# Performance work log

Measured on AMD Instinct MI355X. Metric: run time of the kernel, lower is better.

The kernel has to match this reference:

```python
import jax, jax.numpy as jnp
import numpy as np
import math

D_MODEL = 128
N_HEADS = 8
D_K = D_MODEL // N_HEADS
D_FF = 512
N_LAYERS = 3
N_BUCKETS = 32
EPS = 1e-5
NEG_INF = -1e9
SCALE = 1.0 / math.sqrt(D_K)


def _hier_adj_np(N, L=8):
    # deterministic hierarchical edges from ExpanderGraphBuilder.build_hierarchical_edges
    stride = max(1, int(math.sqrt(N / L)))
    layer_size = N // L if L <= N else 1
    A = np.zeros((N, N), dtype=np.float32)
    for l in range(min(L, N)):
        start = l * layer_size
        end = min(start + layer_size, N)
        for i in range(start, end):
            A[i, max(start, i - stride):min(end, i + stride + 1)] = 1.0
            A[i, i] = 0.0
    return np.maximum(A, A.T)


def _build_mask(h, depot_idx=0):
    # h: (B,N,D). Returns additive mask (B,N+1,N+1) incl. global node.
    B, N, _ = h.shape
    k = min(max(1, math.ceil(math.log2(N))), N - 1)
    sq = jnp.sum(h * h, axis=-1)
    d2 = sq[:, :, None] + sq[:, None, :] - 2.0 * jnp.einsum('bnd,bmd->bnm', h, h)
    d2 = d2 + jnp.where(jnp.eye(N, dtype=bool), jnp.inf, 0.0)
    _, knn_idx = jax.lax.top_k(-d2, k)  # (B,N,k) nearest neighbors
    b_ix = jnp.arange(B)[:, None, None]
    i_ix = jnp.arange(N)[None, :, None]
    adj = jnp.zeros((B, N, N), dtype=h.dtype).at[b_ix, i_ix, knn_idx].set(1.0)
    adj = jnp.maximum(adj, adj.transpose(0, 2, 1))  # symmetrize knn
    adj = jnp.maximum(adj, jnp.asarray(_hier_adj_np(N))[None])
    adj = adj.at[:, depot_idx, :].set(1.0)
    adj = adj.at[:, :, depot_idx].set(1.0)
    adj = jnp.maximum(adj, jnp.eye(N, dtype=h.dtype)[None])
    full = jnp.ones((B, N + 1, N + 1), dtype=h.dtype).at[:, :N, :N].set(adj)
    return jnp.where(full > 0, 0.0, NEG_INF).astype(h.dtype)


def _inorm(x, w, b):
    # InstanceNorm1d over node dim per channel (x: (B,N1,D))
    mu = jnp.mean(x, axis=1, keepdims=True)
    var = jnp.mean(jnp.square(x - mu), axis=1, keepdims=True)
    return (x - mu) * jax.lax.rsqrt(var + EPS) * w + b


def _ega_layer(hg, bucket, mask, Wq, Wk, Wv, Wo, emb, W1, b1, W2, b2, n1w, n1b, n2w, n2b):
    B, N1, D = hg.shape
    heads = lambda x: x.reshape(B, N1, N_HEADS, D_K).transpose(0, 2, 1, 3)
    Q, K, V = heads(hg @ Wq.T), heads(hg @ Wk.T), heads(hg @ Wv.T)
    scores = jnp.einsum('bhnd,bhmd->bhnm', Q, K) * SCALE
    # rel_scores[b,h,i,j] = <Q[b,h,i], emb[bucket[b,i,j], h]> : contract with the
    # 32-entry table first, then gather - same math, no (B,H,N,N,Dk) intermediate.
    qe = jnp.einsum('bhnd,khd->bhnk', Q, emb.reshape(N_BUCKETS, N_HEADS, D_K))
    rel = jnp.take_along_axis(qe, jnp.broadcast_to(bucket[:, None], (B, N_HEADS, N1, N1)), axis=3)
    attn = jax.nn.softmax(scores + rel + mask[:, None], axis=-1)
    ctx = jnp.einsum('bhnm,bhmd->bhnd', attn, V).transpose(0, 2, 1, 3).reshape(B, N1, D)
    h1 = _inorm(hg + ctx @ Wo.T, n1w, n1b)
    ffn = jax.nn.relu(h1 @ W1.T + b1) @ W2.T + b2
    return _inorm(h1 + ffn, n2w, n2b)


def _forward(coords, in_W, in_b, gnode, Wq, Wk, Wv, Wo, emb, W1, b1, W2, b2,
             n1_w, n1_b, n2_w, n2_b, out_W, out_b):
    B, N, _ = coords.shape
    h = coords @ in_W.T + in_b
    g = jnp.broadcast_to(gnode, (B, 1, D_MODEL)).astype(h.dtype)
    # distance buckets over coords extended with the global node at (0,0)
    coords_ext = jnp.concatenate([coords, jnp.zeros((B, 1, 2), coords.dtype)], axis=1)
    diff = coords_ext[:, :, None, :] - coords_ext[:, None, :, :]
    dist = jax.lax.stop_gradient(jnp.sqrt(jnp.sum(diff * diff, axis=-1)))
    bucket = jnp.clip((dist * N_BUCKETS).astype(jnp.int32), 0, N_BUCKETS - 1)  # (B,N+1,N+1)
    pools = []
    for l in range(N_LAYERS):
        g = g + h.mean(axis=1, keepdims=True)
        hg = jnp.concatenate([h, g], axis=1)
        mask = _build_mask(jax.lax.stop_gradient(h))  # torch builds adj via .item(): detached
        hg = _ega_layer(hg, bucket, mask, Wq[l], Wk[l], Wv[l], Wo[l], emb[l],
                        W1[l], b1[l], W2[l], b2[l], n1_w[l], n1_b[l], n2_w[l], n2_b[l])
        h, g = hg[:, :N], hg[:, N:]
        pools.append(h.mean(axis=1))
    p_multi = jnp.stack(pools, axis=1).mean(axis=1)
    E_static = (h + p_multi[:, None, :]) @ out_W.T + out_b
    return E_static, p_multi


def setup_inputs():
    key = jax.random.key(0)
    ks = jax.random.split(key, 24)
    B, N, L = 2, 1024, N_LAYERS
    def nrm(k, shape, s=0.05):
        return jax.random.normal(k, shape, dtype=jnp.float32) * s
    return {
        'coords': jax.random.uniform(ks[0], (B, N, 2), dtype=jnp.float32),
        'in_W': nrm(ks[1], (D_MODEL, 2), 0.5),
        'in_b': nrm(ks[2], (D_MODEL,)),
        'gnode': nrm(ks[3], (1, 1, D_MODEL), 0.2),
        'Wq': nrm(ks[4], (L, D_MODEL, D_MODEL)),
        'Wk': nrm(ks[5], (L, D_MODEL, D_MODEL)),
        'Wv': nrm(ks[6], (L, D_MODEL, D_MODEL)),
        'Wo': nrm(ks[7], (L, D_MODEL, D_MODEL)),
        'emb': nrm(ks[8], (L, N_BUCKETS, N_HEADS * D_K)),
        'W1': nrm(ks[9], (L, D_FF, D_MODEL)),
        'b1': nrm(ks[10], (L, D_FF)),
        'W2': nrm(ks[11], (L, D_MODEL, D_FF)),
        'b2': nrm(ks[12], (L, D_MODEL)),
        'n1_w': jnp.ones((L, D_MODEL), jnp.float32) + nrm(ks[13], (L, D_MODEL)),
        'n1_b': nrm(ks[14], (L, D_MODEL)),
        'n2_w': jnp.ones((L, D_MODEL), jnp.float32) + nrm(ks[15], (L, D_MODEL)),
        'n2_b': nrm(ks[16], (L, D_MODEL)),
        'out_W': nrm(ks[17], (D_MODEL, D_MODEL)),
        'out_b': nrm(ks[18], (D_MODEL,)),
    }


def reference(coords, in_W, in_b, gnode, Wq, Wk, Wv, Wo, emb, W1, b1, W2, b2,
              n1_w, n1_b, n2_w, n2_b, out_W, out_b):
    return _forward(coords, in_W, in_b, gnode, Wq, Wk, Wv, Wo, emb, W1, b1, W2, b2,
                    n1_w, n1_b, n2_w, n2_b, out_W, out_b)
```

## Files before the change

### kernel.cpp

```cpp
#include <hip/hip_runtime.h>

#define BB 2
#define NN 1024
#define N1 1025
#define DM 128
#define NH 8
#define DK 16
#define DFF 512
#define NBUK 32
#define NLAYERS 3
#define KNN_K 10
#define ADJW 17
#define BSTR 1088
#define NSPLIT 8
#define BIGF 3.0e38f
#define SM_OFF 24.0f

#define PWQ_OFF 0
#define PWK_OFF 49152
#define PWV_OFF 98304
#define PWO_OFF 147456
#define PW1_OFF 196608
#define PW2_OFF 393216
#define PWOUT_OFF 589824
#define PWQE_OFF 606208
#define PW_TOT 704512

#define PBLK 344
#define NBNODE 1024
#define EBLK (NBNODE + BB)
#define BBLK 8713

#define KSEL_BLK 512
#define QKV_GX 33
#define QKV_BLK (QKV_GX * 40)
#define OSUM_N (BB * NH * N1 * 16)
#define LSUM_N (BB * NH * N1)
#define STAT_N (BB * DM)
#define ZTOT (OSUM_N + LSUM_N + 2 * STAT_N)

typedef __attribute__((ext_vector_type(8))) short bf8;
typedef __attribute__((ext_vector_type(4))) float f4;
typedef unsigned short u16;
typedef unsigned int u32;

__device__ __forceinline__ u16 f2bf(float x) {
  unsigned u = __float_as_uint(x);
  return (u16)((u + 0x7fff + ((u >> 16) & 1)) >> 16);
}
__device__ __forceinline__ float bf2f(u16 u) {
  return __uint_as_float(((unsigned)u) << 16);
}
__device__ __forceinline__ bf8 mk8(ushort4 a, ushort4 b) {
  bf8 r;
  r[0] = (short)a.x; r[1] = (short)a.y; r[2] = (short)a.z; r[3] = (short)a.w;
  r[4] = (short)b.x; r[5] = (short)b.y; r[6] = (short)b.z; r[7] = (short)b.w;
  return r;
}

__global__ __launch_bounds__(256) void init_kernel(
    const float* __restrict__ coords, const float* __restrict__ inW,
    const float* __restrict__ inb, const float* __restrict__ gnode,
    const float* __restrict__ Wq, const float* __restrict__ Wk,
    const float* __restrict__ Wv, const float* __restrict__ Wo,
    const float* __restrict__ W1, const float* __restrict__ W2,
    const float* __restrict__ oW, const float* __restrict__ emb,
    u16* __restrict__ PH, u16* __restrict__ PL,
    float* __restrict__ X, u16* __restrict__ XH, u16* __restrict__ XM,
    u16* __restrict__ XL, unsigned char* __restrict__ buckp) {
  int blk = blockIdx.x;
  if (blk < PBLK) {
    int idx = blk * 256 + threadIdx.x;
    if (idx >= 88064) return;
    if (idx >= 75776) {
      int rel = idx - 75776;
      int lane = rel & 63, g = rel >> 6;
      int ks = g & 3, nt = g >> 2;
      int n = nt * 16 + (lane & 15);
      int k = ks * 32 + (lane >> 4) * 8;
      int l = n >> 8; int c = n & 255; int h = c >> 5, bk = c & 31;
      const float* e = emb + ((size_t)l * NBUK + bk) * DM + h * DK;
      const float* wq = Wq + ((size_t)l * DM + h * DK) * DM;
      u16* ph = PH + (size_t)idx * 8;
      u16* pl = PL + (size_t)idx * 8;
      #pragma unroll
      for (int q = 0; q < 8; ++q) {
        float s = 0.f;
        #pragma unroll
        for (int d = 0; d < DK; ++d) s += e[d] * wq[(size_t)d * DM + k + q];
        u16 hh = f2bf(s);
        ph[q] = hh;
        pl[q] = f2bf(s - bf2f(hh));
      }
      return;
    }
    const float* W; int rel, Kdim;
    if (idx < 24576) {
      int seg = idx / 6144; rel = idx % 6144; Kdim = 128;
      W = seg == 0 ? Wq : seg == 1 ? Wk : seg == 2 ? Wv : Wo;
    } else if (idx < 49152) { rel = idx - 24576; Kdim = 128; W = W1; }
    else if (idx < 73728)   { rel = idx - 49152; Kdim = 512; W = W2; }
    else                    { rel = idx - 73728; Kdim = 128; W = oW; }
    int lane = rel & 63;
    int g = rel >> 6;
    int ksteps = Kdim >> 5;
    int ks = g % ksteps, nt = g / ksteps;
    int n = nt * 16 + (lane & 15);
    int k = ks * 32 + (lane >> 4) * 8;
    const float* p = W + (size_t)n * Kdim + k;
    u16* ph = PH + (size_t)idx * 8;
    u16* pl = PL + (size_t)idx * 8;
    #pragma unroll
    for (int q = 0; q < 8; ++q) {
      float x = p[q];
      u16 hh = f2bf(x);
      ph[q] = hh;
      pl[q] = f2bf(x - bf2f(hh));
    }
    return;
  }
  if (blk < PBLK + EBLK) {
    int eb = blk - PBLK;
    if (eb >= NBNODE) {
      int b = eb - NBNODE;
      int t = threadIdx.x;
      if (t >= 128) return;
      int lane = t & 63;
      float sx = 0.f, sy = 0.f;
      for (int n = lane; n < NN; n += 64) {
        float2 c = *(const float2*)(coords + (size_t)(b * NN + n) * 2);
        sx += c.x; sy += c.y;
      }
      #pragma unroll
      for (int o = 1; o < 64; o <<= 1) { sx += __shfl_xor(sx, o); sy += __shfl_xor(sy, o); }
      float mx = sx * (1.0f / NN), my = sy * (1.0f / NN);
      int d = t;
      size_t id = ((size_t)b * N1 + NN) * DM + d;
      float v = gnode[d] + inb[d] + mx * inW[d * 2 + 0] + my * inW[d * 2 + 1];
      X[id] = v;
      u16 hh = f2bf(v); float r1 = v - bf2f(hh);
      u16 mm = f2bf(r1);
      XH[id] = hh; XM[id] = mm; XL[id] = f2bf(r1 - bf2f(mm));
      return;
    }
    int idx = eb * 256 + threadIdx.x;
    if (idx >= BB * NN * DM) return;
    int d = idx % DM; int r = idx / DM; int n = r % NN; int b = r / NN;
    float cx = coords[(b * NN + n) * 2 + 0], cy = coords[(b * NN + n) * 2 + 1];
    size_t id = ((size_t)b * N1 + n) * DM + d;
    float v = cx * inW[d * 2 + 0] + cy * inW[d * 2 + 1] + inb[d];
    X[id] = v;
    u16 hh = f2bf(v); float r1 = v - bf2f(hh);
    u16 mm = f2bf(r1);
    XH[id] = hh; XM[id] = mm; XL[id] = f2bf(r1 - bf2f(mm));
    return;
  }
  int idx = (blk - PBLK - EBLK) * 256 + threadIdx.x;
  if (idx >= BB * N1 * BSTR) return;
  int j = idx % BSTR; int r = idx / BSTR; int i = r % N1; int b = r / N1;
  unsigned char v = 0;
  if (j < N1) {
    float xi = 0.f, yi = 0.f, xj = 0.f, yj = 0.f;
    if (i < NN) { xi = coords[(b * NN + i) * 2]; yi = coords[(b * NN + i) * 2 + 1]; }
    if (j < NN) { xj = coords[(b * NN + j) * 2]; yj = coords[(b * NN + j) * 2 + 1]; }
    float dx = xi - xj, dy = yi - yj;
    float dist = sqrtf(dx * dx + dy * dy);
    int bu = (int)(dist * 32.0f);
    bu = bu < 0 ? 0 : (bu > 31 ? 31 : bu);
    v = (unsigned char)bu;
  }
  buckp[idx] = v;
}

__global__ __launch_bounds__(256) void gram_kernel(
    const u16* __restrict__ XH, const u16* __restrict__ XM, const u16* __restrict__ XL,
    unsigned long long* __restrict__ adj, float* __restrict__ d2) {
  __shared__ __align__(16) u16 AsH[32][72];
  __shared__ __align__(16) u16 AsM[32][72];
  __shared__ __align__(16) u16 AsL[32][72];
  __shared__ __align__(16) u16 BsH[64][72];
  __shared__ __align__(16) u16 BsM[64][72];
  __shared__ __align__(16) u16 BsL[64][72];
  __shared__ float sqS[64];
  int b = blockIdx.z;
  int m0 = blockIdx.x * 32, n0 = blockIdx.y * 64;
  size_t boff = (size_t)b * N1;
  int t = threadIdx.x;

  {
    int flat = blockIdx.x + 32 * (blockIdx.y + 16 * blockIdx.z);
    int tid = flat * 256 + t;
    if (tid < BB * N1 * ADJW) adj[tid] = 0ull;
  }

  int lane = t & 63, w = t >> 6;
  int wm = (w >> 1) * 16, wn = (w & 1) * 32;
  int quad = lane >> 4, r16 = lane & 15;

  f4 acc0 = {0.f, 0.f, 0.f, 0.f}, acc1 = {0.f, 0.f, 0.f, 0.f};
  int ar = t >> 3, as_ = (t & 7) * 8;
  int br = t >> 2, bs_ = (t & 3) * 16;
  int sqrow = t >> 2, sqk = (t & 3) * 16;
  float mySq = 0.f;

  for (int k0 = 0; k0 < DM; k0 += 64) {
    {
      size_t src = (boff + m0 + ar) * DM + k0 + as_;
      *(bf8*)&AsH[ar][as_] = *(const bf8*)(XH + src);
      *(bf8*)&AsM[ar][as_] = *(const bf8*)(XM + src);
      *(bf8*)&AsL[ar][as_] = *(const bf8*)(XL + src);
    }
    {
      size_t src = (boff + n0 + br) * DM + k0 + bs_;
      *(bf8*)&BsH[br][bs_] = *(const bf8*)(XH + src);
      *(bf8*)&BsH[br][bs_ + 8] = *(const bf8*)(XH + src + 8);
      *(bf8*)&BsM[br][bs_] = *(const bf8*)(XM + src);
      *(bf8*)&BsM[br][bs_ + 8] = *(const bf8*)(XM + src + 8);
      *(bf8*)&BsL[br][bs_] = *(const bf8*)(XL + src);
      *(bf8*)&BsL[br][bs_ + 8] = *(const bf8*)(XL + src + 8);
    }
    __syncthreads();
    #pragma unroll
    for (int ks = 0; ks < 64; ks += 16) {
      int seg = (quad & 1) * 8;
      bf8 aHM = *(const bf8*)((quad < 2) ? &AsH[wm + r16][ks + seg] : &AsM[wm + r16][ks + seg]);
      bf8 aHL = *(const bf8*)((quad < 2) ? &AsH[wm + r16][ks + seg] : &AsL[wm + r16][ks + seg]);
      #pragma unroll
      for (int tt = 0; tt < 2; ++tt) {
        int nr = wn + tt * 16 + r16;
        bf8 bH = *(const bf8*)&BsH[nr][ks + seg];
        bf8 bM = *(const bf8*)&BsM[nr][ks + seg];
        bf8 b3 = *(const bf8*)((quad < 2) ? &BsL[nr][ks + seg] : &BsH[nr][ks + seg]);
        f4& a = tt ? acc1 : acc0;
        a = __builtin_amdgcn_mfma_f32_16x16x32_bf16(aHM, bH, a, 0, 0, 0);
        a = __builtin_amdgcn_mfma_f32_16x16x32_bf16(aHM, bM, a, 0, 0, 0);
        a = __builtin_amdgcn_mfma_f32_16x16x32_bf16(aHL, b3, a, 0, 0, 0);
      }
    }
    #pragma unroll
    for (int half = 0; half < 2; ++half) {
      bf8 hv = *(const bf8*)&BsH[sqrow][sqk + half * 8];
      bf8 mv = *(const bf8*)&BsM[sqrow][sqk + half * 8];
      bf8 lv = *(const bf8*)&BsL[sqrow][sqk + half * 8];
      #pragma unroll
      for (int q = 0; q < 8; ++q) {
        float x = (bf2f((u16)hv[q]) + bf2f((u16)mv[q])) + bf2f((u16)lv[q]);
        mySq += x * x;
      }
    }
    __syncthreads();
  }
  mySq += __shfl_xor(mySq, 1);
  mySq += __shfl_xor(mySq, 2);
  if ((t & 3) == 0) sqS[sqrow] = mySq;
  __syncthreads();

  #pragma unroll
  for (int tt = 0; tt < 2; ++tt) {
    f4 a = tt ? acc1 : acc0;
    int nl = wn + tt * 16 + r16;
    int n = n0 + nl;
    float sj = sqS[nl];
    #pragma unroll
    for (int reg = 0; reg < 4; ++reg) {
      int m = m0 + wm + quad * 4 + reg;
      float v = (m == n) ? BIGF : (sj - 2.f * a[reg]);
      d2[((size_t)b * NN + m) * NN + n] = v;
    }
  }
}

__global__ __launch_bounds__(256) void knnqkv_kernel(
    const float* __restrict__ d2, unsigned long long* __restrict__ adj,
    const u16* __restrict__ AH, const u16* __restrict__ AL,
    const u16* __restrict__ Pbase_H, const u16* __restrict__ Pbase_L,
    size_t offQ, size_t offK, size_t offV, size_t offE,
    u16* __restrict__ QH, u16* __restrict__ QL,
    u16* __restrict__ KH, u16* __restrict__ KL, u16* __restrict__ Vbf,
    float* __restrict__ qe_all, float* __restrict__ zbuf, int M) {
  __shared__ float dd[4][NN];
  {
    int ztid = blockIdx.x * 256 + threadIdx.x;
    if (ztid < ZTOT) zbuf[ztid] = 0.f;
  }
  int blk = blockIdx.x;
  if (blk < KSEL_BLK) {
    int b = blk / (NN / 4);
    int i0 = (blk % (NN / 4)) * 4;
    int t = threadIdx.x, lane = t & 63, w = t >> 6;

    const float4* src = (const float4*)(d2 + ((size_t)b * NN + i0) * NN);
    float4* dst = (float4*)&dd[0][0];
    #pragma unroll
    for (int x = 0; x < 4; ++x) dst[t + x * 256] = src[t + x * 256];
    __syncthreads();

    int i = i0 + w;
    for (int it = 0; it < KNN_K; ++it) {
      float bv = BIGF; int bi = 0x3fffffff;
      for (int j = lane; j < NN; j += 64) {
        float v = dd[w][j];
        if (v < bv) { bv = v; bi = j; }
      }
      #pragma unroll
      for (int o = 1; o < 64; o <<= 1) {
        float ov = __shfl_xor(bv, o); int oi = __shfl_xor(bi, o);
        if (ov < bv || (ov == bv && oi < bi)) { bv = ov; bi = oi; }
      }
      if (lane == 0) {
        dd[w][bi] = BIGF;
        atomicOr(&adj[((size_t)b * N1 + i) * ADJW + (bi >> 6)], 1ull << (bi & 63));
        atomicOr(&adj[((size_t)b * N1 + bi) * ADJW + (i >> 6)], 1ull << (i & 63));
      }
    }
    return;
  }
  int rel = blk - KSEL_BLK;
  int gx = rel % QKV_GX;
  int y = rel / QKV_GX;
  int z, nt;
  if (y < 8) { z = 0; nt = y; }
  else if (y < 16) { z = 1; nt = y - 8; }
  else if (y < 24) { z = 2; nt = y - 16; }
  else { z = 3; nt = y - 24; }
  size_t woff = z == 0 ? offQ : (z == 1 ? offK : (z == 2 ? offV : offE));
  const u16* PH = Pbase_H + woff;
  const u16* PL = Pbase_L + woff;
  int lane = threadIdx.x & 63;
  int quad = lane >> 4, r16 = lane & 15;
  int mt = gx * 4 + (threadIdx.x >> 6);
  f4 acc = {0.f, 0.f, 0.f, 0.f};
  int m0 = mt * 16;
  int mrow = m0 + r16; if (mrow >= M) mrow = M - 1;
  const u16* aph = AH + (size_t)mrow * DM + quad * 8;
  const u16* apl = AL + (size_t)mrow * DM + quad * 8;
  const u16* ph = PH + ((size_t)nt * 4 * 64 + lane) * 8;
  const u16* pl = PL + ((size_t)nt * 4 * 64 + lane) * 8;
  #pragma unroll
  for (int ks = 0; ks < 4; ++ks) {
    bf8 aH = *(const bf8*)(aph);
    bf8 aL = *(const bf8*)(apl);
    aph += 32; apl += 32;
    bf8 bH = *(const bf8*)(ph + (size_t)ks * 512);
    bf8 bL = *(const bf8*)(pl + (size_t)ks * 512);
    acc = __builtin_amdgcn_mfma_f32_16x16x32_bf16(aH, bH, acc, 0, 0, 0);
    acc = __builtin_amdgcn_mfma_f32_16x16x32_bf16(aH, bL, acc, 0, 0, 0);
    acc = __builtin_amdgcn_mfma_f32_16x16x32_bf16(aL, bH, acc, 0, 0, 0);
  }
  if (m0 >= M) return;
  int n = nt * 16 + r16;
  #pragma unroll
  for (int reg = 0; reg < 4; ++reg) {
    int m = m0 + quad * 4 + reg;
    if (m >= M) continue;
    float v = acc[reg];
    if (z == 3) {
      int b = m / N1, nr = m % N1;
      int h = n >> 5, bk = n & 31;
      qe_all[(((size_t)b * NH + h) * N1 + nr) * 32 + bk] = v;
      continue;
    }
    size_t oi = (size_t)m * DM + n;
    if (z == 0) {
      float sv = v * 0.25f;
      u16 hh = f2bf(sv);
      QH[oi] = hh;
      QL[oi] = f2bf(sv - bf2f(hh));
    } else if (z == 1) {
      u16 hh = f2bf(v);
      KH[oi] = hh;
      KL[oi] = f2bf(v - bf2f(hh));
    } else {
      Vbf[oi] = f2bf(v);
    }
  }
}

__global__ __launch_bounds__(256) void gemm_wo_kernel(
    const float* __restrict__ Osum, const float* __restrict__ lsum,
    const u16* __restrict__ PH, const u16* __restrict__ PL,
    const float* __restrict__ res, float* __restrict__ outF,
    float* __restrict__ sumY, float* __restrict__ sumY2, int M) {
  __shared__ float sA[2][16], sQ[2][16];
  int t = threadIdx.x;
  if (t < 32) {
    sA[t >> 4][t & 15] = 0.f;
    sQ[t >> 4][t & 15] = 0.f;
  }
  __syncthreads();
  int lane = t & 63;
  int quad = lane >> 4, r16 = lane & 15;
  int mt = blockIdx.x * 4 + (t >> 6), nt = blockIdx.y;
  f4 acc = {0.f, 0.f, 0.f, 0.f};
  int m0 = mt * 16;
  int mrow = m0 + r16; if (mrow >= M) mrow = M - 1;
  int b = mrow / N1, nr = mrow % N1;
  const u16* ph = PH + ((size_t)nt * 4 * 64 + lane) * 8;
  const u16* pl = PL + ((size_t)nt * 4 * 64 + lane) * 8;
  #pragma unroll
  for (int ks = 0; ks < 4; ++ks) {
    int k = ks * 32 + quad * 8;
    int h = k >> 4, d0 = k & 15;
    size_t base = (size_t)(b * NH + h) * N1 + nr;
    float inv = 1.0f / lsum[base];
    const float* op = Osum + base * 16 + d0;
    bf8 aH, aL;
    #pragma unroll
    for (int j = 0; j < 8; ++j) {
      float v = op[j] * inv;
      u16 hh = f2bf(v);
      aH[j] = (short)hh;
      aL[j] = (short)f2bf(v - bf2f(hh));
    }
    bf8 bH = *(const bf8*)(ph + (size_t)ks * 512);
    bf8 bL = *(const bf8*)(pl + (size_t)ks * 512);
    acc = __builtin_amdgcn_mfma_f32_16x16x32_bf16(aH, bH, acc, 0, 0, 0);
    acc = __builtin_amdgcn_mfma_f32_16x16x32_bf16(aH, bL, acc, 0, 0, 0);
    acc = __builtin_amdgcn_mfma_f32_16x16x32_bf16(aL, bH, acc, 0, 0, 0);
  }
  int n = nt * 16 + r16;
  if (m0 < M) {
    #pragma unroll
    for (int reg = 0; reg < 4; ++reg) {
      int m = m0 + quad * 4 + reg;
      if (m < M) {
        float v = acc[reg] + res[(size_t)m * DM + n];
        outF[(size_t)m * DM + n] = v;
        int mb2 = m / N1;
        atomicAdd(&sA[mb2][r16], v);
        atomicAdd(&sQ[mb2][r16], v * v);
      }
    }
  }
  __syncthreads();
  if (t < 32) {
    int bb = t >> 4, d = nt * 16 + (t & 15);
    atomicAdd(&sumY[bb * DM + d], sA[bb][t & 15]);
    atomicAdd(&sumY2[bb * DM + d], sQ[bb][t & 15]);
  }
}

__global__ __launch_bounds__(256) void gemm_w1_kernel(
    const float* __restrict__ Yb, const float* __restrict__ sumY,
    const float* __restrict__ sumY2, const float* __restrict__ n1w,
    const float* __restrict__ n1b,
    const u16* __restrict__ PH, const u16* __restrict__ PL,
    const float* __restrict__ bias,
    u16* __restrict__ outH, u16* __restrict__ outL, int M) {
  __shared__ float muS[STAT_N], scvS[STAT_N], shS[STAT_N];
  int t = threadIdx.x;
  {
    float mu = sumY[t] * (1.0f / N1);
    float var = sumY2[t] * (1.0f / N1) - mu * mu;
    int d = t & (DM - 1);
    muS[t] = mu;
    scvS[t] = rsqrtf(var + 1e-5f) * n1w[d];
    shS[t] = n1b[d];
  }
  __syncthreads();
  int lane = t & 63;
  int quad = lane >> 4, r16 = lane & 15;
  int mt = blockIdx.x * 4 + (t >> 6), nt = blockIdx.y;
  f4 acc = {0.f, 0.f, 0.f, 0.f};
  int m0 = mt * 16;
  int mrow = m0 + r16; if (mrow >= M) mrow = M - 1;
  int b = mrow / N1;
  const float* yp = Yb + (size_t)mrow * DM + quad * 8;
  const u16* ph = PH + ((size_t)nt * 4 * 64 + lane) * 8;
  const u16* pl = PL + ((size_t)nt * 4 * 64 + lane) * 8;
  #pragma unroll
  for (int ks = 0; ks < 4; ++ks) {
    int k = ks * 32 + quad * 8;
    bf8 aH, aL;
    #pragma unroll
    for (int half = 0; half < 2; ++half) {
      float4 yv = *(const float4*)(yp + ks * 32 + half * 4);
      float ya[4] = {yv.x, yv.y, yv.z, yv.w};
      #pragma unroll
      for (int q = 0; q < 4; ++q) {
        int sidx = b * DM + k + half * 4 + q;
        float nv = (ya[q] - muS[sidx]) * scvS[sidx] + shS[sidx];
        u16 hh = f2bf(nv);
        aH[half * 4 + q] = (short)hh;
        aL[half * 4 + q] = (short)f2bf(nv - bf2f(hh));
      }
    }
    bf8 bH = *(const bf8*)(ph + (size_t)ks * 512);
    bf8 bL = *(const bf8*)(pl + (size_t)ks * 512);
    acc = __builtin_amdgcn_mfma_f32_16x16x32_bf16(aH, bH, acc, 0, 0, 0);
    acc = __builtin_amdgcn_mfma_f32_16x16x32_bf16(aH, bL, acc, 0, 0, 0);
    acc = __builtin_amdgcn_mfma_f32_16x16x32_bf16(aL, bH, acc, 0, 0, 0);
  }
  if (m0 >= M) return;
  int n = nt * 16 + r16;
  #pragma unroll
  for (int reg = 0; reg < 4; ++reg) {
    int m = m0 + quad * 4 + reg;
    if (m < M) {
      float v = fmaxf(acc[reg] + bias[n], 0.f);
      size_t oi = (size_t)m * DFF + n;
      u16 hh = f2bf(v);
      outH[oi] = hh;
      outL[oi] = f2bf(v - bf2f(hh));
    }
  }
}

__global__ __launch_bounds__(256) void gemm_w2_kernel(
    const u16* __restrict__ AH, const u16* __restrict__ AL,
    const u16* __restrict__ PH, const u16* __restrict__ PL,
    const float* __restrict__ bias, const float* __restrict__ Yb,
    const float* __restrict__ sumY, const float* __restrict__ sumY2,
    const float* __restrict__ n1w, const float* __restrict__ n1b,
    float* __restrict__ outF, int M) {
  __shared__ float muS[STAT_N], scvS[STAT_N], shS[STAT_N];
  int t = threadIdx.x;
  {
    float mu = sumY[t] * (1.0f / N1);
    float var = sumY2[t] * (1.0f / N1) - mu * mu;
    int d = t & (DM - 1);
    muS[t] = mu;
    scvS[t] = rsqrtf(var + 1e-5f) * n1w[d];
    shS[t] = n1b[d];
  }
  __syncthreads();
  int lane = t & 63;
  int quad = lane >> 4, r16 = lane & 15;
  int mt = blockIdx.x * 4 + (t >> 6), nt = blockIdx.y;
  f4 acc = {0.f, 0.f, 0.f, 0.f};
  int m0 = mt * 16;
  int mrow = m0 + r16; if (mrow >= M) mrow = M - 1;
  const u16* aph = AH + (size_t)mrow * DFF + quad * 8;
  const u16* apl = AL + (size_t)mrow * DFF + quad * 8;
  const u16* ph = PH + ((size_t)nt * 16 * 64 + lane) * 8;
  const u16* pl = PL + ((size_t)nt * 16 * 64 + lane) * 8;
  #pragma unroll 4
  for (int ks = 0; ks < 16; ++ks) {
    bf8 aH = *(const bf8*)(aph);
    bf8 aL = *(const bf8*)(apl);
    aph += 32; apl += 32;
    bf8 bH = *(const bf8*)(ph + (size_t)ks * 512);
    bf8 bL = *(const bf8*)(pl + (size_t)ks * 512);
    acc = __builtin_amdgcn_mfma_f32_16x16x32_bf16(aH, bH, acc, 0, 0, 0);
    acc = __builtin_amdgcn_mfma_f32_16x16x32_bf16(aH, bL, acc, 0, 0, 0);
    acc = __builtin_amdgcn_mfma_f32_16x16x32_bf16(aL, bH, acc, 0, 0, 0);
  }
  if (m0 >= M) return;
  int n = nt * 16 + r16;
  #pragma unroll
  for (int reg = 0; reg < 4; ++reg) {
    int m = m0 + quad * 4 + reg;
    if (m < M) {
      int b = m / N1;
      int sidx = b * DM + n;
      float h1 = (Yb[(size_t)m * DM + n] - muS[sidx]) * scvS[sidx] + shS[sidx];
      outF[(size_t)m * DM + n] = acc[reg] + bias[n] + h1;
    }
  }
}

#define CH 64
#define NCH 17
__global__ __launch_bounds__(128) void attn_kernel(
    const u16* __restrict__ QH, const u16* __restrict__ QL,
    const u16* __restrict__ KH, const u16* __restrict__ KL,
    const u16* __restrict__ Vbf, const float* __restrict__ qe_all,
    const unsigned char* __restrict__ buckp, const unsigned long long* __restrict__ adj,
    float* __restrict__ Osum, float* __restrict__ lsum) {
  __shared__ __align__(16) u16 KsHi[2][CH][20];
  __shared__ __align__(16) u16 KsLo[2][CH][20];
  __shared__ __align__(16) u16 Vt[2][DK][68];
  __shared__ __align__(16) u16 Ps[2][16][72];
  __shared__ __align__(16) float qe_s[2][16][36];
  __shared__ u32 maskS[32][6];
  __shared__ unsigned char buckS[2][32][68];

  int qt = blockIdx.x;
  int h = blockIdx.y & 7, b = blockIdx.y >> 3;
  int s = blockIdx.z;
  int c0 = (NCH * s) / NSPLIT, c1 = (NCH * (s + 1)) / NSPLIT;
  int nwm = 2 * (c1 - c0);
  int t = threadIdx.x, lane = t & 63, w = t >> 6;
  int quad = lane >> 4, r16 = lane & 15;
  int i0 = qt * 32;
  int iw = i0 + w * 16;
  int bh = b * NH + h;

  for (int x = t; x < 32 * nwm; x += 128) {
    int rr = x / nwm, ww = x % nwm;
    int gi = i0 + rr; if (gi > NN) gi = NN;
    int W = 2 * c0 + ww;
    u32 v;
    if (gi == 0 || gi == NN) {
      v = 0xffffffffu;
    } else {
      const u32* a32 = (const u32*)(adj + ((size_t)b * N1 + gi) * ADJW);
      v = a32[W];
      int bs = gi & ~127;
      int lo = gi - 11 < bs ? bs : gi - 11;
      int be = bs + 127;
      int hi = gi + 11 > be ? be : gi + 11;
      int aa = lo - 32 * W, bnd = hi - 32 * W;
      if (aa < 0) aa = 0; if (bnd > 31) bnd = 31;
      if (aa <= bnd) v |= (0xffffffffu << aa) & (0xffffffffu >> (31 - bnd));
      if (W == 0) v |= 1u;
      if (W == 32) v |= 1u;
      int dg = gi - 32 * W;
      if (dg >= 0 && dg < 32) v |= 1u << dg;
    }
    if (W == 32) v &= 1u;
    else if (W == 33) v = 0u;
    maskS[rr][ww] = v;
  }
  #pragma unroll
  for (int e = 0; e < 2; ++e) {
    int x = lane + e * 64;
    int rr = x >> 3, bk = (x & 7) * 4;
    int gi = iw + rr; if (gi > NN) gi = NN;
    f4 v = *(const f4*)(qe_all + (((size_t)b * NH + h) * N1 + gi) * 32 + bk);
    *(f4*)&qe_s[w][rr][bk] = v;
  }
  bf8 qfrag;
  {
    int gi = iw + r16; if (gi > NN) gi = NN;
    const u16* qsrc = (quad < 2 ? QH : QL) + ((size_t)(b * N1 + gi) * DM + h * DK + (quad & 1) * 8);
    qfrag = *(const bf8*)qsrc;
  }

  ushort4 khr[2], klr[2], vvr[2]; u32 bkr[4];
  auto load_chunk = [&](int c) {
    int j0 = c * CH;
    #pragma unroll
    for (int ii = 0; ii < 2; ++ii) {
      int x = t + ii * 128;
      int key = x >> 2, ds = (x & 3) * 4;
      int jg = j0 + key; if (jg > NN) jg = NN;
      size_t src = (size_t)(b * N1 + jg) * DM + h * DK + ds;
      khr[ii] = *(const ushort4*)(KH + src);
      klr[ii] = *(const ushort4*)(KL + src);
      vvr[ii] = *(const ushort4*)(Vbf + src);
    }
    #pragma unroll
    for (int ii = 0; ii < 4; ++ii) {
      int x = t + ii * 128;
      int rr = x >> 4, c4 = (x & 15) * 4;
      int gi = i0 + rr; if (gi > NN) gi = NN;
      bkr[ii] = *(const u32*)(buckp + ((size_t)b * N1 + gi) * BSTR + j0 + c4);
    }
  };
  auto store_chunk = [&](int pb) {
    #pragma unroll
    for (int ii = 0; ii < 2; ++ii) {
      int x = t + ii * 128;
      int key = x >> 2, ds = (x & 3) * 4;
      *(ushort4*)&KsHi[pb][key][ds] = khr[ii];
      *(ushort4*)&KsLo[pb][key][ds] = klr[ii];
      Vt[pb][ds + 0][key] = vvr[ii].x;
      Vt[pb][ds + 1][key] = vvr[ii].y;
      Vt[pb][ds + 2][key] = vvr[ii].z;
      Vt[pb][ds + 3][key] = vvr[ii].w;
    }
    #pragma unroll
    for (int ii = 0; ii < 4; ++ii) {
      int x = t + ii * 128;
      int rr = x >> 4, c4 = (x & 15) * 4;
      *(u32*)&buckS[pb][rr][c4] = bkr[ii];
    }
  };

  f4 Oacc = {0.f, 0.f, 0.f, 0.f};
  float lrun[4] = {0.f, 0.f, 0.f, 0.f};

  load_chunk(c0);
  store_chunk(0);

  for (int c = c0; c < c1; ++c) {
    int pb = (c - c0) & 1;
    bool pf = (c + 1 < c1);
    if (pf) load_chunk(c + 1);
    __syncthreads();

    f4 S[4];
    #pragma unroll
    for (int tt = 0; tt < 4; ++tt) {
      int key = tt * 16 + r16;
      int off = (quad & 1) * 8;
      bf8 bhv = mk8(*(const ushort4*)&KsHi[pb][key][off], *(const ushort4*)&KsHi[pb][key][off + 4]);
      bf8 blv = mk8(*(const ushort4*)&KsLo[pb][key][off], *(const ushort4*)&KsLo[pb][key][off + 4]);
      f4 z = {0.f, 0.f, 0.f, 0.f};
      z = __builtin_amdgcn_mfma_f32_16x16x32_bf16(qfrag, bhv, z, 0, 0, 0);
      z = __builtin_amdgcn_mfma_f32_16x16x32_bf16(qfrag, blv, z, 0, 0, 0);
      S[tt] = z;
    }

    #pragma unroll
    for (int rg = 0; rg < 4; ++rg) {
      int rowb = w * 16 + quad * 4 + rg;
      u32 mw0 = maskS[rowb][2 * (c - c0)];
      u32 mw1 = maskS[rowb][2 * (c - c0) + 1];
      float ps = 0.f;
      #pragma unroll
      for (int tt = 0; tt < 4; ++tt) {
        u32 mword = (tt & 2) ? mw1 : mw0;
        int bit = (tt & 1) * 16 + r16;
        int bk = buckS[pb][rowb][tt * 16 + r16] & 31;
        float rel = qe_s[w][quad * 4 + rg][bk];
        float sc = S[tt][rg] + rel;
        sc += ((mword >> bit) & 1u) ? 0.f : -1.0e9f;
        float p = __expf(sc - SM_OFF);
        ps += p;
        Ps[w][quad * 4 + rg][tt * 16 + r16] = f2bf(p);
      }
      #pragma unroll
      for (int o = 1; o < 16; o <<= 1) ps += __shfl_xor(ps, o);
      lrun[rg] += ps;
    }
    #pragma unroll
    for (int half = 0; half < 2; ++half) {
      bf8 pa = *(const bf8*)&Ps[w][r16][half * 32 + quad * 8];
      bf8 vb = mk8(*(const ushort4*)&Vt[pb][r16][half * 32 + quad * 8],
                   *(const ushort4*)&Vt[pb][r16][half * 32 + quad * 8 + 4]);
      Oacc = __builtin_amdgcn_mfma_f32_16x16x32_bf16(pa, vb, Oacc, 0, 0, 0);
    }

    if (pf) store_chunk(pb ^ 1);
  }

  #pragma unroll
  for (int rg = 0; rg < 4; ++rg) {
    int gi = i0 + w * 16 + quad * 4 + rg;
    if (gi < N1) {
      size_t base = (size_t)bh * N1 + gi;
      atomicAdd(&Osum[base * 16 + r16], Oacc[rg]);
      if (r16 == 0) atomicAdd(&lsum[base], lrun[rg]);
    }
  }
}

__global__ void inorm_kernel(float* __restrict__ X, const float* __restrict__ w,
                             const float* __restrict__ b_, float* __restrict__ pool,
                             int do_g, u16* __restrict__ oH, u16* __restrict__ oM,
                             u16* __restrict__ oL) {
  int d = blockIdx.x; int bb = blockIdx.y; int lane = threadIdx.x;
  float g_old = X[((size_t)bb * N1 + NN) * DM + d];
  float s = 0.f;
  for (int n = lane; n < N1; n += 64) s += X[((size_t)bb * N1 + n) * DM + d];
  #pragma unroll
  for (int o = 1; o < 64; o <<= 1) s += __shfl_xor(s, o);
  float mu = s * (1.0f / N1);
  float v = 0.f;
  for (int n = lane; n < N1; n += 64) {
    float tt = X[((size_t)bb * N1 + n) * DM + d] - mu;
    v += tt * tt;
  }
  #pragma unroll
  for (int o = 1; o < 64; o <<= 1) v += __shfl_xor(v, o);
  float var = v * (1.0f / N1);
  float scv = rsqrtf(var + 1e-5f) * w[d];
  float sh = b_[d];
  for (int n = lane; n < N1; n += 64) {
    size_t id = ((size_t)bb * N1 + n) * DM + d;
    float nv = (X[id] - mu) * scv + sh;
    X[id] = nv;
    if (oH) {
      u16 hh = f2bf(nv); float r1 = nv - bf2f(hh);
      u16 mm = f2bf(r1);
      oH[id] = hh;
      oM[id] = mm;
      if (oL) oL[id] = f2bf(r1 - bf2f(mm));
    }
  }
  if (lane == 0) {
    float hmean = ((s - g_old) * (1.0f / NN) - mu) * scv + sh;
    if (pool) pool[bb * DM + d] = hmean;
    if (do_g) X[((size_t)bb * N1 + NN) * DM + d] += hmean;
  }
}

__global__ __launch_bounds__(256) void gemm_final_kernel(
    const float* __restrict__ X, const float* __restrict__ pools,
    const u16* __restrict__ PH, const u16* __restrict__ PL,
    const float* __restrict__ bias, float* __restrict__ out, float* __restrict__ out_pm) {
  int t = threadIdx.x;
  if (blockIdx.x == 0 && blockIdx.y == 0) {
    float pmv = (pools[t] + pools[BB * DM + t] + pools[2 * BB * DM + t]) * (1.0f / 3.0f);
    out_pm[t] = pmv;
  }
  int lane = t & 63;
  int quad = lane >> 4, r16 = lane & 15;
  int mt = blockIdx.x * 4 + (t >> 6), nt = blockIdx.y;
  const int M = BB * NN;
  f4 acc = {0.f, 0.f, 0.f, 0.f};
  int m0 = mt * 16;
  int mrow = m0 + r16; if (mrow >= M) mrow = M - 1;
  int mb = mrow / NN, mn = mrow % NN;
  const float* xp = X + ((size_t)mb * N1 + mn) * DM + quad * 8;
  const float* pp = pools + mb * DM + quad * 8;
  const u16* ph = PH + ((size_t)nt * 4 * 64 + lane) * 8;
  const u16* pl = PL + ((size_t)nt * 4 * 64 + lane) * 8;
  #pragma unroll
  for (int ks = 0; ks < 4; ++ks) {
    bf8 aH, aL;
    #pragma unroll
    for (int half = 0; half < 2; ++half) {
      float4 xv = *(const float4*)(xp + ks * 32 + half * 4);
      float4 p0 = *(const float4*)(pp + ks * 32 + half * 4);
      float4 p1 = *(const float4*)(pp + BB * DM + ks * 32 + half * 4);
      float4 p2 = *(const float4*)(pp + 2 * BB * DM + ks * 32 + half * 4);
      float av[4] = {xv.x + (p0.x + p1.x + p2.x) * (1.0f / 3.0f),
                     xv.y + (p0.y + p1.y + p2.y) * (1.0f / 3.0f),
                     xv.z + (p0.z + p1.z + p2.z) * (1.0f / 3.0f),
                     xv.w + (p0.w + p1.w + p2.w) * (1.0f / 3.0f)};
      #pragma unroll
      for (int q = 0; q < 4; ++q) {
        u16 hh = f2bf(av[q]);
        aH[half * 4 + q] = (short)hh;
        aL[half * 4 + q] = (short)f2bf(av[q] - bf2f(hh));
      }
    }
    bf8 bH = *(const bf8*)(ph + (size_t)ks * 512);
    bf8 bL = *(const bf8*)(pl + (size_t)ks * 512);
    acc = __builtin_amdgcn_mfma_f32_16x16x32_bf16(aH, bH, acc, 0, 0, 0);
    acc = __builtin_amdgcn_mfma_f32_16x16x32_bf16(aH, bL, acc, 0, 0, 0);
    acc = __builtin_amdgcn_mfma_f32_16x16x32_bf16(aL, bH, acc, 0, 0, 0);
  }
  int n = nt * 16 + r16;
  #pragma unroll
  for (int reg = 0; reg < 4; ++reg) {
    int m = m0 + quad * 4 + reg;
    if (m < M) out[(size_t)m * DM + n] = acc[reg] + bias[n];
  }
}

extern "C" void kernel_launch(void* const* d_in, const int* in_sizes, int n_in,
                              void* d_out, int out_size, void* d_ws, size_t ws_size,
                              hipStream_t stream) {
  const float* coords = (const float*)d_in[0];
  const float* inW    = (const float*)d_in[1];
  const float* inb    = (const float*)d_in[2];
  const float* gnode  = (const float*)d_in[3];
  const float* Wq     = (const float*)d_in[4];
  const float* Wk     = (const float*)d_in[5];
  const float* Wv     = (const float*)d_in[6];
  const float* Wo     = (const float*)d_in[7];
  const float* emb    = (const float*)d_in[8];
  const float* W1     = (const float*)d_in[9];
  const float* b1     = (const float*)d_in[10];
  const float* W2     = (const float*)d_in[11];
  const float* b2     = (const float*)d_in[12];
  const float* n1w    = (const float*)d_in[13];
  const float* n1b    = (const float*)d_in[14];
  const float* n2w    = (const float*)d_in[15];
  const float* n2b    = (const float*)d_in[16];
  const float* outW   = (const float*)d_in[17];
  const float* outb   = (const float*)d_in[18];
  float* out = (float*)d_out;

  char* wsp = (char*)d_ws;
  size_t off = 0;
  auto alloc = [&](size_t bytes) -> void* {
    off = (off + 255) & ~(size_t)255;
    void* p = wsp + off;
    off += bytes;
    return p;
  };
  const size_t XB = (size_t)BB * N1 * DM * 4;
  const size_t HB = (size_t)BB * N1 * DM * 2;
  float* X0   = (float*)alloc(XB);
  float* X1   = (float*)alloc(XB);
  float* Yb   = (float*)alloc(XB);
  u16* XH = (u16*)alloc(HB); u16* XM = (u16*)alloc(HB); u16* XL = (u16*)alloc(HB);
  u16* QH = (u16*)alloc(HB); u16* QL = (u16*)alloc(HB);
  u16* KH = (u16*)alloc(HB); u16* KL = (u16*)alloc(HB);
  u16* Vbf = (u16*)alloc(HB);
  u16* FbH = (u16*)alloc((size_t)BB * N1 * DFF * 2);
  u16* FbL = (u16*)alloc((size_t)BB * N1 * DFF * 2);
  unsigned char* buckp = (unsigned char*)alloc((size_t)BB * N1 * BSTR);
  unsigned long long* adj = (unsigned long long*)alloc((size_t)BB * N1 * ADJW * 8);
  float* pools = (float*)alloc((size_t)NLAYERS * BB * DM * 4);
  float* qe_all = (float*)alloc((size_t)BB * NH * N1 * 32 * 4);
  float* zbuf = (float*)alloc((size_t)ZTOT * 4);
  u16* PH = (u16*)alloc((size_t)PW_TOT * 2);
  u16* PL = (u16*)alloc((size_t)PW_TOT * 2);
  float* d2 = (float*)alloc((size_t)BB * NN * NN * 4);

  float* Osum = zbuf;
  float* lsum = zbuf + OSUM_N;
  float* sumY = zbuf + OSUM_N + LSUM_N;
  float* sumY2 = sumY + STAT_N;

  init_kernel<<<PBLK + EBLK + BBLK, 256, 0, stream>>>(
      coords, inW, inb, gnode, Wq, Wk, Wv, Wo, W1, W2, outW, emb,
      PH, PL, X0, XH, XM, XL, buckp);

  float* Xin = X0; float* Xout = X1;
  const int M = BB * N1;
  const int GX = 33;
  for (int l = 0; l < NLAYERS; ++l) {
    gram_kernel<<<dim3(32, 16, BB), 256, 0, stream>>>(XH, XM, XL, adj, d2);

    knnqkv_kernel<<<KSEL_BLK + QKV_BLK, 256, 0, stream>>>(
        d2, adj, XH, XM, PH, PL,
        (size_t)PWQ_OFF + (size_t)l * DM * DM,
        (size_t)PWK_OFF + (size_t)l * DM * DM,
        (size_t)PWV_OFF + (size_t)l * DM * DM,
        (size_t)PWQE_OFF + (size_t)l * 256 * DM,
        QH, QL, KH, KL, Vbf, qe_all, zbuf, M);

    attn_kernel<<<dim3(33, NH * BB, NSPLIT), 128, 0, stream>>>(
        QH, QL, KH, KL, Vbf, qe_all, buckp, adj, Osum, lsum);

    gemm_wo_kernel<<<dim3(GX, 8), 256, 0, stream>>>(
        Osum, lsum, PH + PWO_OFF + (size_t)l * DM * DM, PL + PWO_OFF + (size_t)l * DM * DM,
        Xin, Yb, sumY, sumY2, M);

    gemm_w1_kernel<<<dim3(GX, 32), 256, 0, stream>>>(
        Yb, sumY, sumY2, n1w + l * DM, n1b + l * DM,
        PH + PW1_OFF + (size_t)l * DFF * DM, PL + PW1_OFF + (size_t)l * DFF * DM,
        b1 + l * DFF, FbH, FbL, M);

    gemm_w2_kernel<<<dim3(GX, 8), 256, 0, stream>>>(
        FbH, FbL, PH + PW2_OFF + (size_t)l * DM * DFF, PL + PW2_OFF + (size_t)l * DM * DFF,
        b2 + l * DM, Yb, sumY, sumY2, n1w + l * DM, n1b + l * DM, Xout, M);

    inorm_kernel<<<dim3(DM, BB), 64, 0, stream>>>(Xout, n2w + l * DM, n2b + l * DM,
                                                  pools + (size_t)l * BB * DM, 1,
                                                  XH, XM, XL);

    float* t2 = Xin; Xin = Xout; Xout = t2;
  }

  gemm_final_kernel<<<dim3(32, 8), 256, 0, stream>>>(
      Xin, pools, PH + PWOUT_OFF, PL + PWOUT_OFF, outb, out, out + (size_t)BB * NN * DM);
}
```

Before: 422.3 us.

## Fuse second InstanceNorm statistics into W2 GEMM epilogue and elementwise apply kernel

```diff
diff --git a/kernel.cpp b/kernel.cpp
--- a/kernel.cpp
+++ b/kernel.cpp
@@ -37,7 +37,7 @@
 #define OSUM_N (BB * NH * N1 * 16)
 #define LSUM_N (BB * NH * N1)
 #define STAT_N (BB * DM)
-#define ZTOT (OSUM_N + LSUM_N + 2 * STAT_N)
+#define ZTOT (OSUM_N + LSUM_N + 4 * STAT_N)
 
 typedef __attribute__((ext_vector_type(8))) short bf8;
 typedef __attribute__((ext_vector_type(4))) float f4;
@@ -512,8 +512,10 @@
     const float* __restrict__ bias, const float* __restrict__ Yb,
     const float* __restrict__ sumY, const float* __restrict__ sumY2,
     const float* __restrict__ n1w, const float* __restrict__ n1b,
-    float* __restrict__ outF, int M) {
+    float* __restrict__ outF, float* __restrict__ sumX, float* __restrict__ sumX2,
+    float* __restrict__ gsave, int M) {
   __shared__ float muS[STAT_N], scvS[STAT_N], shS[STAT_N];
+  __shared__ float sA[2][16], sQ[2][16];
   int t = threadIdx.x;
   {
     float mu = sumY[t] * (1.0f / N1);
@@ -522,6 +524,10 @@
     muS[t] = mu;
     scvS[t] = rsqrtf(var + 1e-5f) * n1w[d];
     shS[t] = n1b[d];
+  }
+  if (t < 32) {
+    sA[t >> 4][t & 15] = 0.f;
+    sQ[t >> 4][t & 15] = 0.f;
   }
   __syncthreads();
   int lane = t & 63;
@@ -545,18 +551,53 @@
     acc = __builtin_amdgcn_mfma_f32_16x16x32_bf16(aH, bL, acc, 0, 0, 0);
     acc = __builtin_amdgcn_mfma_f32_16x16x32_bf16(aL, bH, acc, 0, 0, 0);
   }
-  if (m0 >= M) return;
   int n = nt * 16 + r16;
-  #pragma unroll
-  for (int reg = 0; reg < 4; ++reg) {
-    int m = m0 + quad * 4 + reg;
-    if (m < M) {
-      int b = m / N1;
-      int sidx = b * DM + n;
-      float h1 = (Yb[(size_t)m * DM + n] - muS[sidx]) * scvS[sidx] + shS[sidx];
-      outF[(size_t)m * DM + n] = acc[reg] + bias[n] + h1;
-    }
-  }
+  if (m0 < M) {
+    #pragma unroll
+    for (int reg = 0; reg < 4; ++reg) {
+      int m = m0 + quad * 4 + reg;
+      if (m < M) {
+        int b = m / N1, mn2 = m % N1;
+        int sidx = b * DM + n;
+        float h1 = (Yb[(size_t)m * DM + n] - muS[sidx]) * scvS[sidx] + shS[sidx];
+        float v = acc[reg] + bias[n] + h1;
+        outF[(size_t)m * DM + n] = v;
+        atomicAdd(&sA[b][r16], v);
+        atomicAdd(&sQ[b][r16], v * v);
+        if (mn2 == NN) gsave[sidx] = v;
+      }
+    }
+  }
+  __syncthreads();
+  if (t < 32) {
+    int bb = t >> 4, d = nt * 16 + (t & 15);
+    atomicAdd(&sumX[bb * DM + d], sA[bb][t & 15]);
+    atomicAdd(&sumX2[bb * DM + d], sQ[bb][t & 15]);
+  }
+}
+
+__global__ __launch_bounds__(256) void xsplit2_kernel(
+    float* __restrict__ X, const float* __restrict__ sumX, const float* __restrict__ sumX2,
+    const float* __restrict__ gsave, const float* __restrict__ w, const float* __restrict__ b_,
+    float* __restrict__ pool, u16* __restrict__ XH, u16* __restrict__ XM,
+    u16* __restrict__ XL) {
+  int idx = blockIdx.x * 256 + threadIdx.x;
+  if (idx >= BB * N1 * DM) return;
+  int d = idx % DM; int r = idx / DM; int n = r % N1; int b = r / N1;
+  int sidx = b * DM + d;
+  float sx = sumX[sidx];
+  float mu = sx * (1.0f / N1);
+  float var = sumX2[sidx] * (1.0f / N1) - mu * mu;
+  float scv = rsqrtf(var + 1e-5f) * w[d];
+  float sh = b_[d];
+  float hmean = ((sx - gsave[sidx]) * (1.0f / NN) - mu) * scv + sh;
+  float nv = (X[idx] - mu) * scv + sh;
+  if (n == NN) nv += hmean;
+  X[idx] = nv;
+  u16 hh = f2bf(nv); float r1 = nv - bf2f(hh);
+  u16 mm = f2bf(r1);
+  XH[idx] = hh; XM[idx] = mm; XL[idx] = f2bf(r1 - bf2f(mm));
+  if (n == 0) pool[sidx] = hmean;
 }
 
 #define CH 64
@@ -737,55 +778,28 @@
   }
 }
 
-__global__ void inorm_kernel(float* __restrict__ X, const float* __restrict__ w,
-                             const float* __restrict__ b_, float* __restrict__ pool,
-                             int do_g, u16* __restrict__ oH, u16* __restrict__ oM,
-                             u16* __restrict__ oL) {
-  int d = blockIdx.x; int bb = blockIdx.y; int lane = threadIdx.x;
-  float g_old = X[((size_t)bb * N1 + NN) * DM + d];
-  float s = 0.f;
-  for (int n = lane; n < N1; n += 64) s += X[((size_t)bb * N1 + n) * DM + d];
-  #pragma unroll
-  for (int o = 1; o < 64; o <<= 1) s += __shfl_xor(s, o);
-  float mu = s * (1.0f / N1);
-  float v = 0.f;
-  for (int n = lane; n < N1; n += 64) {
-    float tt = X[((size_t)bb * N1 + n) * DM + d] - mu;
-    v += tt * tt;
-  }
-  #pragma unroll
-  for (int o = 1; o < 64; o <<= 1) v += __shfl_xor(v, o);
-  float var = v * (1.0f / N1);
-  float scv = rsqrtf(var + 1e-5f) * w[d];
-  float sh = b_[d];
-  for (int n = lane; n < N1; n += 64) {
-    size_t id = ((size_t)bb * N1 + n) * DM + d;
-    float nv = (X[id] - mu) * scv + sh;
-    X[id] = nv;
-    if (oH) {
-      u16 hh = f2bf(nv); float r1 = nv - bf2f(hh);
-      u16 mm = f2bf(r1);
-      oH[id] = hh;
-      oM[id] = mm;
-      if (oL) oL[id] = f2bf(r1 - bf2f(mm));
-    }
-  }
-  if (lane == 0) {
-    float hmean = ((s - g_old) * (1.0f / NN) - mu) * scv + sh;
-    if (pool) pool[bb * DM + d] = hmean;
-    if (do_g) X[((size_t)bb * N1 + NN) * DM + d] += hmean;
-  }
-}
-
 __global__ __launch_bounds__(256) void gemm_final_kernel(
-    const float* __restrict__ X, const float* __restrict__ pools,
+    const float* __restrict__ X, const float* __restrict__ sumX,
+    const float* __restrict__ sumX2, const float* __restrict__ gsave,
+    const float* __restrict__ n2w, const float* __restrict__ n2b,
+    const float* __restrict__ pools,
     const u16* __restrict__ PH, const u16* __restrict__ PL,
     const float* __restrict__ bias, float* __restrict__ out, float* __restrict__ out_pm) {
+  __shared__ float muS[STAT_N], scvS[STAT_N], shS[STAT_N], pmS[STAT_N];
   int t = threadIdx.x;
-  if (blockIdx.x == 0 && blockIdx.y == 0) {
-    float pmv = (pools[t] + pools[BB * DM + t] + pools[2 * BB * DM + t]) * (1.0f / 3.0f);
-    out_pm[t] = pmv;
-  }
+  {
+    float sx = sumX[t];
+    float mu = sx * (1.0f / N1);
+    float var = sumX2[t] * (1.0f / N1) - mu * mu;
+    int d = t & (DM - 1);
+    float scv = rsqrtf(var + 1e-5f) * n2w[d];
+    float sh = n2b[d];
+    float hmean = ((sx - gsave[t]) * (1.0f / NN) - mu) * scv + sh;
+    float pm = (pools[t] + pools[BB * DM + t] + hmean) * (1.0f / 3.0f);
+    muS[t] = mu; scvS[t] = scv; shS[t] = sh; pmS[t] = pm;
+    if (blockIdx.x == 0 && blockIdx.y == 0) out_pm[t] = pm;
+  }
+  __syncthreads();
   int lane = t & 63;
   int quad = lane >> 4, r16 = lane & 15;
   int mt = blockIdx.x * 4 + (t >> 6), nt = blockIdx.y;
@@ -795,27 +809,23 @@
   int mrow = m0 + r16; if (mrow >= M) mrow = M - 1;
   int mb = mrow / NN, mn = mrow % NN;
   const float* xp = X + ((size_t)mb * N1 + mn) * DM + quad * 8;
-  const float* pp = pools + mb * DM + quad * 8;
   const u16* ph = PH + ((size_t)nt * 4 * 64 + lane) * 8;
   const u16* pl = PL + ((size_t)nt * 4 * 64 + lane) * 8;
   #pragma unroll
   for (int ks = 0; ks < 4; ++ks) {
+    int k = ks * 32 + quad * 8;
     bf8 aH, aL;
     #pragma unroll
     for (int half = 0; half < 2; ++half) {
       float4 xv = *(const float4*)(xp + ks * 32 + half * 4);
-      float4 p0 = *(const float4*)(pp + ks * 32 + half * 4);
-      float4 p1 = *(const float4*)(pp + BB * DM + ks * 32 + half * 4);
-      float4 p2 = *(const float4*)(pp + 2 * BB * DM + ks * 32 + half * 4);
-      float av[4] = {xv.x + (p0.x + p1.x + p2.x) * (1.0f / 3.0f),
-                     xv.y + (p0.y + p1.y + p2.y) * (1.0f / 3.0f),
-                     xv.z + (p0.z + p1.z + p2.z) * (1.0f / 3.0f),
-                     xv.w + (p0.w + p1.w + p2.w) * (1.0f / 3.0f)};
+      float xa[4] = {xv.x, xv.y, xv.z, xv.w};
       #pragma unroll
       for (int q = 0; q < 4; ++q) {
-        u16 hh = f2bf(av[q]);
+        int sidx = mb * DM + k + half * 4 + q;
+        float av = (xa[q] - muS[sidx]) * scvS[sidx] + shS[sidx] + pmS[sidx];
+        u16 hh = f2bf(av);
         aH[half * 4 + q] = (short)hh;
-        aL[half * 4 + q] = (short)f2bf(av[q] - bf2f(hh));
+        aL[half * 4 + q] = (short)f2bf(av - bf2f(hh));
       }
     }
     bf8 bH = *(const bf8*)(ph + (size_t)ks * 512);
@@ -880,6 +890,7 @@
   float* pools = (float*)alloc((size_t)NLAYERS * BB * DM * 4);
   float* qe_all = (float*)alloc((size_t)BB * NH * N1 * 32 * 4);
   float* zbuf = (float*)alloc((size_t)ZTOT * 4);
+  float* gsave = (float*)alloc((size_t)STAT_N * 4);
   u16* PH = (u16*)alloc((size_t)PW_TOT * 2);
   u16* PL = (u16*)alloc((size_t)PW_TOT * 2);
   float* d2 = (float*)alloc((size_t)BB * NN * NN * 4);
@@ -888,6 +899,8 @@
   float* lsum = zbuf + OSUM_N;
   float* sumY = zbuf + OSUM_N + LSUM_N;
   float* sumY2 = sumY + STAT_N;
+  float* sumX = sumY2 + STAT_N;
+  float* sumX2 = sumX + STAT_N;
 
   init_kernel<<<PBLK + EBLK + BBLK, 256, 0, stream>>>(
       coords, inW, inb, gnode, Wq, Wk, Wv, Wo, W1, W2, outW, emb,
@@ -921,15 +934,19 @@
 
     gemm_w2_kernel<<<dim3(GX, 8), 256, 0, stream>>>(
         FbH, FbL, PH + PW2_OFF + (size_t)l * DM * DFF, PL + PW2_OFF + (size_t)l * DM * DFF,
-        b2 + l * DM, Yb, sumY, sumY2, n1w + l * DM, n1b + l * DM, Xout, M);
-
-    inorm_kernel<<<dim3(DM, BB), 64, 0, stream>>>(Xout, n2w + l * DM, n2b + l * DM,
-                                                  pools + (size_t)l * BB * DM, 1,
-                                                  XH, XM, XL);
+        b2 + l * DM, Yb, sumY, sumY2, n1w + l * DM, n1b + l * DM,
+        Xout, sumX, sumX2, gsave, M);
+
+    if (l < NLAYERS - 1) {
+      xsplit2_kernel<<<(BB * N1 * DM + 255) / 256, 256, 0, stream>>>(
+          Xout, sumX, sumX2, gsave, n2w + l * DM, n2b + l * DM,
+          pools + (size_t)l * BB * DM, XH, XM, XL);
+    }
 
     float* t2 = Xin; Xin = Xout; Xout = t2;
   }
 
   gemm_final_kernel<<<dim3(32, 8), 256, 0, stream>>>(
-      Xin, pools, PH + PWOUT_OFF, PL + PWOUT_OFF, outb, out, out + (size_t)BB * NN * DM);
-}
+      Xin, sumX, sumX2, gsave, n2w + 2 * DM, n2b + 2 * DM, pools,
+      PH + PWOUT_OFF, PL + PWOUT_OFF, outb, out, out + (size_t)BB * NN * DM);
+}
```

New measurement: 382.3 us (median of 3 runs). 9.5% less time.
